# Optimization experiments

Measured on AMD Instinct MI355X. Metric: run time of the kernel, lower is better.

Reference implementation:

```python
import jax, jax.numpy as jnp
import numpy as np

B, L = 4, 1024
CS, CP, H, C = 384, 128, 8, 64
PQK, PV, RANK, K = 8, 12, 2, 10
CZ4 = CP // 4
ANG_TO_NM = 0.1
INF = 1e9


def layer_norm(x, g, b):
    m = jnp.mean(x, -1, keepdims=True)
    v = jnp.var(x, -1, keepdims=True)
    return (x - m) * jax.lax.rsqrt(v + 1e-5) * g + b


def quat_to_rot(q):
    w, x, y, z = q[..., 0], q[..., 1], q[..., 2], q[..., 3]
    R = jnp.stack([1 - 2 * (y * y + z * z), 2 * (x * y - w * z), 2 * (x * z + w * y),
                   2 * (x * y + w * z), 1 - 2 * (x * x + z * z), 2 * (y * z - w * x),
                   2 * (x * z - w * y), 2 * (y * z + w * x), 1 - 2 * (x * x + y * y)], -1)
    return R.reshape(q.shape[:-1] + (3, 3))


def pos_emb(n, dim):
    pos = jnp.arange(n, dtype=jnp.float32)[:, None]
    half = dim // 2
    freq = jnp.exp(-np.log(10000.0) / half * jnp.arange(half, dtype=jnp.float32))
    ang = pos * freq[None]
    return jnp.concatenate([jnp.sin(ang), jnp.cos(ang)], -1)


def forward(s, trans, rots, mask, We_s, be_s, We_mlp, be_mlp, Wf1, bf1, Wf2, bf2,
            Wq, Wk, Wv, Wqp, Wkp, Wvp, gamma, Wb1, Wb2, Wz1, Wz2, Wout, bout,
            ln1_g, ln1_b, Wt1, bt1, Wt2, bt2, Wt3, bt3, ln2_g, ln2_b, Wbb, bbb):
    b_, l_ = s.shape[0], s.shape[1]
    # ---- EdgeEmbedder (flash_1d_bias mode): per-node low-rank factors of pair rep,
    # with on-the-fly k-neighbor distance features; never materializes [L,L,c_p]. ----
    node = s @ We_s + be_s                                              # [B,L,CP]
    offs = np.concatenate([np.arange(-K, 0), np.arange(1, K + 1)])      # 2K seq neighbors
    idx = np.clip(np.arange(l_)[None, :] + offs[:, None], 0, l_ - 1)    # [2K,L]
    d = jnp.linalg.norm(trans[:, idx] - trans[:, None], axis=-1)        # [B,2K,L]
    d = jnp.moveaxis(d, 1, 2)                                           # [B,L,2K]
    pe = jnp.broadcast_to(pos_emb(l_, CP)[None], (b_, l_, CP))
    hmid = jax.nn.relu(jnp.concatenate([node, pe, d], -1) @ We_mlp + be_mlp)
    z1 = (hmid @ Wf1 + bf1).reshape(b_, l_, RANK, CP) * mask[..., None, None]
    z2 = (hmid @ Wf2 + bf2).reshape(b_, l_, RANK, CP) * mask[..., None, None]
    # ---- Invariant Point Attention on rigids (translations in nm) ----
    t_nm = trans * ANG_TO_NM
    q = (s @ Wq).reshape(b_, l_, H, C)
    k = (s @ Wk).reshape(b_, l_, H, C)
    v = (s @ Wv).reshape(b_, l_, H, C)
    qp = (s @ Wqp).reshape(b_, l_, H, PQK, 3)
    kp = (s @ Wkp).reshape(b_, l_, H, PQK, 3)
    vp = (s @ Wvp).reshape(b_, l_, H, PV, 3)

    def to_global(p):
        return jnp.einsum('blxy,blhpy->blhpx', rots, p) + t_nm[:, :, None, None, :]

    qp, kp, vp = to_global(qp), to_global(kp), to_global(vp)
    a = jnp.einsum('bihc,bjhc->bhij', q, k) * float(1.0 / np.sqrt(3 * C))
    # factored pair bias: b[h,i,j] = sum_r f1[i,r,h] * f2[j,r,h]
    bf_i = jnp.einsum('birc,ch->birh', z1, Wb1)
    bf_j = jnp.einsum('bjrc,ch->bjrh', z2, Wb2)
    a = a + float(np.sqrt(1.0 / 3.0)) * jnp.einsum('birh,bjrh->bhij', bf_i, bf_j)
    # point attention via |q|^2 + |k|^2 - 2 q.k (no [L,L,P,3] tensor)
    q2 = jnp.moveaxis((qp ** 2).sum((-2, -1)), -1, 1)                   # [B,H,L]
    k2 = jnp.moveaxis((kp ** 2).sum((-2, -1)), -1, 1)
    d2 = q2[..., None] + k2[:, :, None, :] - 2.0 * jnp.einsum('bihpx,bjhpx->bhij', qp, kp)
    head_w = jax.nn.softplus(gamma) * float(np.sqrt(1.0 / (3 * (PQK * 9.0 / 2))))
    a = a - 0.5 * head_w[None, :, None, None] * d2
    a = a + (mask[:, None, None, :] - 1.0) * INF
    a = jax.nn.softmax(a, -1)
    o = jnp.einsum('bhij,bjhc->bihc', a, v).reshape(b_, l_, H * C)
    og = jnp.einsum('bhij,bjhpx->bihpx', a, vp)
    op = jnp.einsum('blyx,blhpy->blhpx', rots, og - t_nm[:, :, None, None, :])
    opn = jnp.sqrt((op ** 2).sum(-1) + 1e-8)                            # [B,L,H,PV]
    # factored pair-value: o_pair[i] = z1v[i] * (a @ z2v)
    zv1 = jnp.einsum('birc,cd->bird', z1, Wz1)
    zv2 = jnp.einsum('bjrc,cd->bjrd', z2, Wz2)
    opair = zv1[:, :, None] * jnp.einsum('bhij,bjrd->bihrd', a, zv2)    # [B,L,H,R,CZ4]
    cat = jnp.concatenate([o, op.reshape(b_, l_, H * PV * 3), opn.reshape(b_, l_, H * PV),
                           opair.reshape(b_, l_, H * RANK * CZ4)], -1)
    s = s + cat @ Wout + bout
    s = layer_norm(s, ln1_g, ln1_b)
    # ---- structure transition (residual MLP + LN) ----
    h2 = jax.nn.relu(s @ Wt1 + bt1)
    h2 = jax.nn.relu(h2 @ Wt2 + bt2)
    s = layer_norm(s + h2 @ Wt3 + bt3, ln2_g, ln2_b)
    # ---- backbone update + rigid compose ----
    u = s @ Wbb + bbb                                                   # [B,L,6]
    quat = jnp.concatenate([jnp.ones(u.shape[:-1] + (1,), u.dtype), u[..., :3]], -1)
    quat = quat / jnp.linalg.norm(quat, axis=-1, keepdims=True)
    r_u = quat_to_rot(quat)
    rots_new = jnp.einsum('blxy,blyz->blxz', rots, r_u)
    trans_new = jnp.einsum('blxy,bly->blx', rots, u[..., 3:]) + trans
    return s, rots_new, trans_new


def setup_inputs() -> dict:
    key = jax.random.key(0)
    ks = jax.random.split(key, 40)

    def w(i, shape, scale=0.02):
        return jax.random.normal(ks[i], shape, jnp.float32) * scale

    s = jax.random.normal(ks[0], (B, L, CS), jnp.float32)
    trans = jax.random.normal(ks[1], (B, L, 3), jnp.float32) * 10.0
    qr = jax.random.normal(ks[2], (B, L, 4), jnp.float32)
    rots = quat_to_rot(qr / jnp.linalg.norm(qr, axis=-1, keepdims=True))
    mask = jnp.ones((B, L), jnp.float32)
    return dict(
        s=s, trans=trans, rots=rots, mask=mask,
        We_s=w(3, (CS, CP)), be_s=jnp.zeros((CP,)),
        We_mlp=w(4, (2 * CP + 2 * K, CP)), be_mlp=jnp.zeros((CP,)),
        Wf1=w(5, (CP, RANK * CP)), bf1=jnp.zeros((RANK * CP,)),
        Wf2=w(6, (CP, RANK * CP)), bf2=jnp.zeros((RANK * CP,)),
        Wq=w(7, (CS, H * C)), Wk=w(8, (CS, H * C)), Wv=w(9, (CS, H * C)),
        Wqp=w(10, (CS, H * PQK * 3)), Wkp=w(11, (CS, H * PQK * 3)), Wvp=w(12, (CS, H * PV * 3)),
        gamma=jnp.zeros((H,)), Wb1=w(13, (CP, H)), Wb2=w(14, (CP, H)),
        Wz1=w(15, (CP, CZ4)), Wz2=w(16, (CP, CZ4)),
        Wout=w(17, (H * (C + PV * 4) + H * RANK * CZ4, CS)), bout=jnp.zeros((CS,)),
        ln1_g=jnp.ones((CS,)), ln1_b=jnp.zeros((CS,)),
        Wt1=w(18, (CS, CS)), bt1=jnp.zeros((CS,)),
        Wt2=w(19, (CS, CS)), bt2=jnp.zeros((CS,)),
        Wt3=w(20, (CS, CS)), bt3=jnp.zeros((CS,)),
        ln2_g=jnp.ones((CS,)), ln2_b=jnp.zeros((CS,)),
        Wbb=w(21, (CS, 6)), bbb=jnp.zeros((6,)))


def reference(s, trans, rots, mask, We_s, be_s, We_mlp, be_mlp, Wf1, bf1, Wf2, bf2,
              Wq, Wk, Wv, Wqp, Wkp, Wvp, gamma, Wb1, Wb2, Wz1, Wz2, Wout, bout,
              ln1_g, ln1_b, Wt1, bt1, Wt2, bt2, Wt3, bt3, ln2_g, ln2_b, Wbb, bbb):
    return forward(s, trans, rots, mask, We_s, be_s, We_mlp, be_mlp, Wf1, bf1, Wf2, bf2,
                   Wq, Wk, Wv, Wqp, Wkp, Wvp, gamma, Wb1, Wb2, Wz1, Wz2, Wout, bout,
                   ln1_g, ln1_b, Wt1, bt1, Wt2, bt2, Wt3, bt3, ln2_g, ln2_b, Wbb, bbb)
```

## Files before the change

### kernel.cpp

```cpp
#include <hip/hip_runtime.h>
#include <math.h>

#define Bb 4
#define Ll 1024
#define CSd 384
#define CPd 128
#define Hh 8
#define BL 4096
#define CAT2W 276
#define CATW 1408
#define QKVW 2208
#define PARTW 168
#define LDP 40

#define S_QK 0.07216878364870322f
#define SQ13 0.5773502691896258f
#define HW_SCALE 0.09622504486493764f

typedef short bf16x8 __attribute__((ext_vector_type(8)));
typedef float f32x4  __attribute__((ext_vector_type(4)));

__device__ __forceinline__ ushort f2bf(float f) {
    uint u = __float_as_uint(f);
    u += 0x7FFF + ((u >> 16) & 1);
    return (ushort)(u >> 16);
}
__device__ __forceinline__ float bf2f(ushort h) {
    return __uint_as_float(((uint)h) << 16);
}

template<bool RELU, bool HASBIAS>
__global__ __launch_bounds__(256) void gemm_mfma(
    const float* __restrict__ A, int lda,
    const float* __restrict__ W, const float* __restrict__ bias,
    float* __restrict__ C, int ldc, int N, int Kd)
{
    __shared__ short Ah[64][LDP], Al[64][LDP];
    __shared__ short Wh[64][LDP], Wl[64][LDP];
    const int tid = threadIdx.x;
    const int lane = tid & 63;
    const int wave = tid >> 6;
    const int qm = wave >> 1, qn = wave & 1;
    const int bm = blockIdx.y * 64, bn = blockIdx.x * 64;

    f32x4 acc[2][2];
#pragma unroll
    for (int i = 0; i < 2; ++i)
#pragma unroll
        for (int j = 0; j < 2; ++j) {
            acc[i][j][0] = 0.f; acc[i][j][1] = 0.f;
            acc[i][j][2] = 0.f; acc[i][j][3] = 0.f;
        }

    const int rsel = lane & 15;
    const int ksel = (lane >> 4) * 8;

    for (int k0 = 0; k0 < Kd; k0 += 32) {
        __syncthreads();
        {
            const int row = tid >> 2, kc = (tid & 3) * 8;
            const float* ap = A + (size_t)(bm + row) * lda + k0 + kc;
            float av[8];
            if (k0 + kc + 8 <= Kd) {
                const float4 a0 = *(const float4*)ap;
                const float4 a1 = *(const float4*)(ap + 4);
                av[0]=a0.x; av[1]=a0.y; av[2]=a0.z; av[3]=a0.w;
                av[4]=a1.x; av[5]=a1.y; av[6]=a1.z; av[7]=a1.w;
            } else {
#pragma unroll
                for (int u = 0; u < 8; ++u)
                    av[u] = (k0 + kc + u < Kd) ? ap[u] : 0.f;
            }
            short hv[8], lv[8];
#pragma unroll
            for (int u = 0; u < 8; ++u) {
                const ushort h = f2bf(av[u]);
                hv[u] = (short)h;
                lv[u] = (short)f2bf(av[u] - bf2f(h));
            }
            *(bf16x8*)&Ah[row][kc] = *(const bf16x8*)hv;
            *(bf16x8*)&Al[row][kc] = *(const bf16x8*)lv;
        }
        {
            const int col = tid & 63, ko = (tid >> 6) * 8;
            const int swz = ((col >> 3) & 3) << 3;
            const bool cok = (bn + col) < N;
            float wv[8];
#pragma unroll
            for (int i = 0; i < 8; ++i) {
                const int k = k0 + ko + i;
                wv[i] = (cok && k < Kd) ? W[(size_t)k * N + bn + col] : 0.f;
            }
            short hv[8], lv[8];
#pragma unroll
            for (int i = 0; i < 8; ++i) {
                const ushort h = f2bf(wv[i]);
                hv[i] = (short)h;
                lv[i] = (short)f2bf(wv[i] - bf2f(h));
            }
            *(bf16x8*)&Wh[col][ko ^ swz] = *(const bf16x8*)hv;
            *(bf16x8*)&Wl[col][ko ^ swz] = *(const bf16x8*)lv;
        }
        __syncthreads();

        bf16x8 afh[2], afl[2], wfh[2], wfl[2];
#pragma unroll
        for (int fr = 0; fr < 2; ++fr) {
            const int row = qm * 32 + fr * 16 + rsel;
            afh[fr] = *(const bf16x8*)&Ah[row][ksel];
            afl[fr] = *(const bf16x8*)&Al[row][ksel];
        }
#pragma unroll
        for (int fc = 0; fc < 2; ++fc) {
            const int col = qn * 32 + fc * 16 + rsel;
            const int swz = ((col >> 3) & 3) << 3;
            wfh[fc] = *(const bf16x8*)&Wh[col][ksel ^ swz];
            wfl[fc] = *(const bf16x8*)&Wl[col][ksel ^ swz];
        }
#pragma unroll
        for (int fr = 0; fr < 2; ++fr)
#pragma unroll
            for (int fc = 0; fc < 2; ++fc) {
                acc[fr][fc] = __builtin_amdgcn_mfma_f32_16x16x32_bf16(
                    afh[fr], wfh[fc], acc[fr][fc], 0, 0, 0);
                acc[fr][fc] = __builtin_amdgcn_mfma_f32_16x16x32_bf16(
                    afh[fr], wfl[fc], acc[fr][fc], 0, 0, 0);
                acc[fr][fc] = __builtin_amdgcn_mfma_f32_16x16x32_bf16(
                    afl[fr], wfh[fc], acc[fr][fc], 0, 0, 0);
            }
    }

#pragma unroll
    for (int fr = 0; fr < 2; ++fr)
#pragma unroll
        for (int fc = 0; fc < 2; ++fc) {
            const int col = bn + qn * 32 + fc * 16 + rsel;
            if (col < N) {
                const float bv = HASBIAS ? bias[col] : 0.f;
#pragma unroll
                for (int r = 0; r < 4; ++r) {
                    const int row = bm + qm * 32 + fr * 16 + (lane >> 4) * 4 + r;
                    float x = acc[fr][fc][r] + bv;
                    if (RELU) x = fmaxf(x, 0.f);
                    C[(size_t)row * ldc + col] = x;
                }
            }
        }
}

__global__ __launch_bounds__(256) void pack_qkv(
    const float* __restrict__ Wq, const float* __restrict__ Wk,
    const float* __restrict__ Wv, const float* __restrict__ Wqp,
    const float* __restrict__ Wkp, const float* __restrict__ Wvp,
    float* __restrict__ Wp)
{
    const int k = blockIdx.x;
    float* dst = Wp + (size_t)k * QKVW;
    for (int n = threadIdx.x; n < QKVW; n += 256) {
        float v;
        if      (n < 512)  v = Wq [(size_t)k*512 + n];
        else if (n < 1024) v = Wk [(size_t)k*512 + n - 512];
        else if (n < 1536) v = Wv [(size_t)k*512 + n - 1024];
        else if (n < 1728) v = Wqp[(size_t)k*192 + n - 1536];
        else if (n < 1920) v = Wkp[(size_t)k*192 + n - 1728];
        else               v = Wvp[(size_t)k*288 + n - 1920];
        dst[n] = v;
    }
}

__global__ __launch_bounds__(256) void pack_f12(
    const float* __restrict__ Wf1, const float* __restrict__ Wf2,
    const float* __restrict__ bf1, const float* __restrict__ bf2,
    float* __restrict__ Wp, float* __restrict__ bp)
{
    const int k = blockIdx.x;
    float* dst = Wp + (size_t)k * 512;
    for (int n = threadIdx.x; n < 512; n += 256)
        dst[n] = (n < 256) ? Wf1[(size_t)k*256 + n] : Wf2[(size_t)k*256 + n - 256];
    if (k == 0)
        for (int n = threadIdx.x; n < 512; n += 256)
            bp[n] = (n < 256) ? bf1[n] : bf2[n - 256];
}

__global__ __launch_bounds__(128) void edge_feat(
    const float* __restrict__ trans, float* __restrict__ cat2)
{
    const int row = blockIdx.x;
    const int l = row & (Ll - 1);
    const int b = row >> 10;
    const int tid = threadIdx.x;
    {
        float v;
        if (tid < 64) {
            const float fr = __expf(-9.210340371976184f / 64.f * (float)tid);
            v = sinf((float)l * fr);
        } else {
            const float fr = __expf(-9.210340371976184f / 64.f * (float)(tid - 64));
            v = cosf((float)l * fr);
        }
        cat2[(size_t)row * CAT2W + 128 + tid] = v;
    }
    if (tid < 20) {
        const int off = (tid < 10) ? (tid - 10) : (tid - 9);
        int j = l + off;
        j = j < 0 ? 0 : (j > Ll - 1 ? Ll - 1 : j);
        const float dx = trans[(size_t)(b*Ll + j)*3 + 0] - trans[(size_t)row*3 + 0];
        const float dy = trans[(size_t)(b*Ll + j)*3 + 1] - trans[(size_t)row*3 + 1];
        const float dz = trans[(size_t)(b*Ll + j)*3 + 2] - trans[(size_t)row*3 + 2];
        cat2[(size_t)row * CAT2W + 256 + tid] = sqrtf(dx*dx + dy*dy + dz*dz);
    }
}

__global__ __launch_bounds__(256) void z_derive(
    const float* __restrict__ z12, const float* __restrict__ mask,
    const float* __restrict__ Wb1, const float* __restrict__ Wb2,
    const float* __restrict__ Wz1, const float* __restrict__ Wz2,
    float* __restrict__ bfi, float* __restrict__ bfj,
    float* __restrict__ zv1, float* __restrict__ zv2)
{
    __shared__ float zsh[512];
    const int row = blockIdx.x;
    const int tid = threadIdx.x;
    for (int idx = tid; idx < 512; idx += 256)
        zsh[idx] = z12[(size_t)row * 512 + idx];
    __syncthreads();
    const float mv = mask[row];
    if (tid < 16) {
        const int r = tid >> 3, h = tid & 7;
        float acc = 0.f;
        for (int c = 0; c < 128; ++c) acc = fmaf(zsh[r*128 + c], Wb1[c*8 + h], acc);
        bfi[(size_t)row*16 + r*8 + h] = mv * acc;
    } else if (tid < 80) {
        const int o = tid - 16, r = o >> 5, dd = o & 31;
        float acc = 0.f;
        for (int c = 0; c < 128; ++c) acc = fmaf(zsh[r*128 + c], Wz1[c*32 + dd], acc);
        zv1[(size_t)row*64 + r*32 + dd] = mv * acc;
    } else if (tid < 96) {
        const int o = tid - 80, r = o >> 3, h = o & 7;
        float acc = 0.f;
        for (int c = 0; c < 128; ++c) acc = fmaf(zsh[256 + r*128 + c], Wb2[c*8 + h], acc);
        bfj[(size_t)row*16 + r*8 + h] = mv * acc;
    } else if (tid < 160) {
        const int o = tid - 96, r = o >> 5, dd = o & 31;
        float acc = 0.f;
        for (int c = 0; c < 128; ++c) acc = fmaf(zsh[256 + r*128 + c], Wz2[c*32 + dd], acc);
        zv2[(size_t)row*64 + r*32 + dd] = mv * acc;
    }
}

__global__ __launch_bounds__(256) void to_global_k(
    const float* __restrict__ rots, const float* __restrict__ trans,
    float* __restrict__ qkv, float* __restrict__ q2, float* __restrict__ k2)
{
    const int row = blockIdx.x;
    const int b = row >> 10, l = row & (Ll - 1);
    const int tid = threadIdx.x;
    __shared__ float sq[64], sk[64];
    float R[9], tn[3];
#pragma unroll
    for (int i = 0; i < 9; ++i) R[i] = rots[(size_t)row*9 + i];
#pragma unroll
    for (int i = 0; i < 3; ++i) tn[i] = trans[(size_t)row*3 + i] * 0.1f;

    float* base = nullptr;
    float* sq2 = nullptr;
    if (tid < 64)       { base = qkv + (size_t)row*QKVW + 1536 + tid*3;        sq2 = &sq[tid]; }
    else if (tid < 128) { base = qkv + (size_t)row*QKVW + 1728 + (tid-64)*3;   sq2 = &sk[tid-64]; }
    else if (tid < 224) { base = qkv + (size_t)row*QKVW + 1920 + (tid-128)*3; }
    if (base) {
        const float px = base[0], py = base[1], pz = base[2];
        const float gx = fmaf(R[0],px, fmaf(R[1],py, fmaf(R[2],pz, tn[0])));
        const float gy = fmaf(R[3],px, fmaf(R[4],py, fmaf(R[5],pz, tn[1])));
        const float gz = fmaf(R[6],px, fmaf(R[7],py, fmaf(R[8],pz, tn[2])));
        base[0] = gx; base[1] = gy; base[2] = gz;
        if (sq2) *sq2 = gx*gx + gy*gy + gz*gz;
    }
    __syncthreads();
    if (tid < 8) {
        float s2 = 0.f;
#pragma unroll
        for (int p = 0; p < 8; ++p) s2 += sq[tid*8 + p];
        q2[((size_t)b*Hh + tid)*Ll + l] = s2;
    } else if (tid < 16) {
        const int h = tid - 8;
        float s2 = 0.f;
#pragma unroll
        for (int p = 0; p < 8; ++p) s2 += sk[h*8 + p];
        k2[((size_t)b*Hh + h)*Ll + l] = s2;
    }
}

__global__ __launch_bounds__(256, 2) void flash_ipa4(
    const float* __restrict__ qkv,
    const float* __restrict__ q2g, const float* __restrict__ k2g,
    const float* __restrict__ bfi, const float* __restrict__ bfj,
    const float* __restrict__ zv2,
    const float* __restrict__ maskg, const float* __restrict__ gamma,
    float* __restrict__ part)
{
    __shared__ float sk[32][64];
    __shared__ float skp[32][32];
    __shared__ float sv[32][64];
    __shared__ float svp[32][36];
    __shared__ float szv[32][64];
    __shared__ float4 sjs[32];

    const int tid = threadIdx.x;
    const int t = tid & 7, g = tid >> 3;
    const int jh = blockIdx.x & 1;
    const int it = (blockIdx.x >> 1) & 7;
    const int bh = blockIdx.x >> 4;
    const int b = bh >> 3, h = bh & 7;
    const int i0 = it * 128 + g;

    const float hw = log1pf(__expf(gamma[h])) * HW_SCALE;
    const float nh = -0.5f * hw;

    float qa[4][8], qp[4][4], cI[4], bfa[4], bfb[4];
#pragma unroll
    for (int rr = 0; rr < 4; ++rr) {
        const int row = b * Ll + i0 + 32 * rr;
        const float* p0 = qkv + (size_t)row * QKVW + h * 64 + 8 * t;
        const float4 a0 = *(const float4*)p0, a1 = *(const float4*)(p0 + 4);
        qa[rr][0]=a0.x*S_QK; qa[rr][1]=a0.y*S_QK; qa[rr][2]=a0.z*S_QK; qa[rr][3]=a0.w*S_QK;
        qa[rr][4]=a1.x*S_QK; qa[rr][5]=a1.y*S_QK; qa[rr][6]=a1.z*S_QK; qa[rr][7]=a1.w*S_QK;
        float4 e0 = make_float4(0,0,0,0);
        if (t < 6)
            e0 = *(const float4*)(qkv + (size_t)row*QKVW + 1536 + h*24 + 4*t);
        qp[rr][0]=e0.x*hw; qp[rr][1]=e0.y*hw; qp[rr][2]=e0.z*hw; qp[rr][3]=e0.w*hw;
        cI[rr]  = nh * q2g[((size_t)b*Hh + h)*Ll + i0 + 32*rr];
        bfa[rr] = SQ13 * bfi[(size_t)row*16 + h];
        bfb[rr] = SQ13 * bfi[(size_t)row*16 + 8 + h];
    }

    float o[4][8] = {}, og[4][5] = {}, op[4][8] = {};
    float m[4] = {-1e30f,-1e30f,-1e30f,-1e30f}, l[4] = {};

    for (int jt = jh * 16; jt < jh * 16 + 16; ++jt) {
        const int rowj = b * Ll + jt * 32;
        __syncthreads();
#pragma unroll
        for (int r = 0; r < 2; ++r) {
            const int idx = tid + 256 * r;
            const int jj = idx >> 4, c4 = idx & 15;
            const float* src = qkv + (size_t)(rowj + jj) * QKVW;
            *(float4*)&sk[jj][c4*4]  = *(const float4*)(src + 512  + h*64 + c4*4);
            *(float4*)&sv[jj][c4*4]  = *(const float4*)(src + 1024 + h*64 + c4*4);
            *(float4*)&szv[jj][c4*4] = *(const float4*)(zv2 + (size_t)(rowj + jj)*64 + c4*4);
        }
        {
            const int jj = tid >> 3, c4 = tid & 7;
            float4 v4 = make_float4(0,0,0,0);
            if (c4 < 6)
                v4 = *(const float4*)(qkv + (size_t)(rowj + jj)*QKVW + 1728 + h*24 + c4*4);
            *(float4*)&skp[jj][c4*4] = v4;
        }
#pragma unroll
        for (int r = 0; r < 2; ++r) {
            const int idx = tid + 256 * r;
            if (idx < 288) {
                const int jj = idx / 9, c4 = idx % 9;
                *(float4*)&svp[jj][c4*4] =
                    *(const float4*)(qkv + (size_t)(rowj + jj)*QKVW + 1920 + h*36 + c4*4);
            }
        }
        if (tid < 32) {
            const int j = jt * 32 + tid;
            sjs[tid] = make_float4(
                k2g[((size_t)b*Hh + h)*Ll + j],
                (maskg[(size_t)b*Ll + j] - 1.f) * 1e9f,
                bfj[(size_t)(b*Ll + j)*16 + h],
                bfj[(size_t)(b*Ll + j)*16 + 8 + h]);
        }
        __syncthreads();

        for (int jj = 0; jj < 32; ++jj) {
            const float4 ka = *(const float4*)&sk[jj][8*t];
            const float4 kb = *(const float4*)&sk[jj][8*t + 4];
            const float4 kp4 = *(const float4*)&skp[jj][4*t];
            const float kv[8] = {ka.x,ka.y,ka.z,ka.w,kb.x,kb.y,kb.z,kb.w};
            const float kpv[4] = {kp4.x,kp4.y,kp4.z,kp4.w};
            float d[4];
#pragma unroll
            for (int rr = 0; rr < 4; ++rr) {
                float dd = 0.f;
#pragma unroll
                for (int u = 0; u < 8; ++u) dd = fmaf(qa[rr][u], kv[u], dd);
#pragma unroll
                for (int u = 0; u < 4; ++u) dd = fmaf(qp[rr][u], kpv[u], dd);
                d[rr] = dd;
            }
#pragma unroll
            for (int rr = 0; rr < 4; ++rr) {
                d[rr] += __shfl_xor(d[rr], 1, 64);
                d[rr] += __shfl_xor(d[rr], 2, 64);
                d[rr] += __shfl_xor(d[rr], 4, 64);
            }
            const float4 js = sjs[jj];

            const float4 va = *(const float4*)&sv[jj][8*t];
            const float4 vb = *(const float4*)&sv[jj][8*t + 4];
            const float vv[8] = {va.x,va.y,va.z,va.w,vb.x,vb.y,vb.z,vb.w};
            const float4 vpa = *(const float4*)&svp[jj][4*t];
            const float vpv[4] = {vpa.x,vpa.y,vpa.z,vpa.w};
            const float vpe = svp[jj][32 + (t & 3)];
            const float vpes = (t < 4) ? vpe : 0.f;
            const float4 za = *(const float4*)&szv[jj][8*t];
            const float4 zb = *(const float4*)&szv[jj][8*t + 4];
            const float zz[8] = {za.x,za.y,za.z,za.w,zb.x,zb.y,zb.z,zb.w};

#pragma unroll
            for (int rr = 0; rr < 4; ++rr) {
                const float lg = d[rr] +
                    fmaf(bfa[rr], js.z, fmaf(bfb[rr], js.w, fmaf(nh, js.x, js.y + cI[rr])));
                if (lg > m[rr]) {
                    const float f = __expf(m[rr] - lg); m[rr] = lg; l[rr] *= f;
#pragma unroll
                    for (int u = 0; u < 8; ++u) o[rr][u] *= f;
#pragma unroll
                    for (int u = 0; u < 5; ++u) og[rr][u] *= f;
#pragma unroll
                    for (int u = 0; u < 8; ++u) op[rr][u] *= f;
                }
                const float p = __expf(lg - m[rr]); l[rr] += p;
#pragma unroll
                for (int u = 0; u < 8; ++u) o[rr][u] = fmaf(p, vv[u], o[rr][u]);
#pragma unroll
                for (int u = 0; u < 4; ++u) og[rr][u] = fmaf(p, vpv[u], og[rr][u]);
                og[rr][4] = fmaf(p, vpes, og[rr][4]);
#pragma unroll
                for (int u = 0; u < 8; ++u) op[rr][u] = fmaf(p, zz[u], op[rr][u]);
            }
        }
    }

#pragma unroll
    for (int rr = 0; rr < 4; ++rr) {
        float* pr = part + ((size_t)(bh * 2 + jh) * Ll + i0 + 32 * rr) * PARTW;
        *(float4*)&pr[8*t]     = make_float4(o[rr][0], o[rr][1], o[rr][2], o[rr][3]);
        *(float4*)&pr[8*t + 4] = make_float4(o[rr][4], o[rr][5], o[rr][6], o[rr][7]);
        *(float4*)&pr[64 + 4*t] = make_float4(og[rr][0], og[rr][1], og[rr][2], og[rr][3]);
        if (t < 4) pr[96 + t] = og[rr][4];
        *(float4*)&pr[100 + 8*t]     = make_float4(op[rr][0], op[rr][1], op[rr][2], op[rr][3]);
        *(float4*)&pr[100 + 8*t + 4] = make_float4(op[rr][4], op[rr][5], op[rr][6], op[rr][7]);
        if (t == 0) { pr[164] = m[rr]; pr[165] = l[rr]; }
    }
}

__global__ __launch_bounds__(256) void combine_ipa(
    const float* __restrict__ part,
    const float* __restrict__ zv1,
    const float* __restrict__ rots, const float* __restrict__ trans,
    float* __restrict__ cat)
{
    __shared__ float sog[64][36];
    const int tid = threadIdx.x;
    const int t = tid & 7, g = tid >> 3;
    const int it = blockIdx.x & 15;
    const int bh = blockIdx.x >> 4;
    const int b = bh >> 3, h = bh & 7;
    const int i0 = it * 64 + g;

#pragma unroll
    for (int rr = 0; rr < 2; ++rr) {
        const int i = i0 + rr * 32;
        const int row = b * Ll + i;
        const float* pA = part + ((size_t)(bh * 2 + 0) * Ll + i) * PARTW;
        const float* pB = part + ((size_t)(bh * 2 + 1) * Ll + i) * PARTW;
        const float mA = pA[164], mB = pB[164];
        const float m = fmaxf(mA, mB);
        const float wA = __expf(mA - m), wB = __expf(mB - m);
        const float l = fmaf(wA, pA[165], wB * pB[165]);
        const float sA = wA / l, sB = wB / l;

        float* crow = cat + (size_t)row * CATW;
        {
            const float4 a0 = *(const float4*)&pA[8*t];
            const float4 a1 = *(const float4*)&pA[8*t + 4];
            const float4 b0 = *(const float4*)&pB[8*t];
            const float4 b1 = *(const float4*)&pB[8*t + 4];
            *(float4*)&crow[h*64 + 8*t] = make_float4(
                fmaf(sA, a0.x, sB * b0.x), fmaf(sA, a0.y, sB * b0.y),
                fmaf(sA, a0.z, sB * b0.z), fmaf(sA, a0.w, sB * b0.w));
            *(float4*)&crow[h*64 + 8*t + 4] = make_float4(
                fmaf(sA, a1.x, sB * b1.x), fmaf(sA, a1.y, sB * b1.y),
                fmaf(sA, a1.z, sB * b1.z), fmaf(sA, a1.w, sB * b1.w));
        }
        {
            const float4 a0 = *(const float4*)&pA[100 + 8*t];
            const float4 a1 = *(const float4*)&pA[100 + 8*t + 4];
            const float4 b0 = *(const float4*)&pB[100 + 8*t];
            const float4 b1 = *(const float4*)&pB[100 + 8*t + 4];
            const float4 z0 = *(const float4*)&zv1[(size_t)row*64 + 8*t];
            const float4 z1 = *(const float4*)&zv1[(size_t)row*64 + 8*t + 4];
            *(float4*)&crow[896 + h*64 + 8*t] = make_float4(
                z0.x * fmaf(sA, a0.x, sB * b0.x), z0.y * fmaf(sA, a0.y, sB * b0.y),
                z0.z * fmaf(sA, a0.z, sB * b0.z), z0.w * fmaf(sA, a0.w, sB * b0.w));
            *(float4*)&crow[896 + h*64 + 8*t + 4] = make_float4(
                z1.x * fmaf(sA, a1.x, sB * b1.x), z1.y * fmaf(sA, a1.y, sB * b1.y),
                z1.z * fmaf(sA, a1.z, sB * b1.z), z1.w * fmaf(sA, a1.w, sB * b1.w));
        }
        {
            const float4 a0 = *(const float4*)&pA[64 + 4*t];
            const float4 b0 = *(const float4*)&pB[64 + 4*t];
            sog[g + rr*32][4*t + 0] = fmaf(sA, a0.x, sB * b0.x);
            sog[g + rr*32][4*t + 1] = fmaf(sA, a0.y, sB * b0.y);
            sog[g + rr*32][4*t + 2] = fmaf(sA, a0.z, sB * b0.z);
            sog[g + rr*32][4*t + 3] = fmaf(sA, a0.w, sB * b0.w);
            if (t < 4)
                sog[g + rr*32][32 + t] = fmaf(sA, pA[96 + t], sB * pB[96 + t]);
        }
    }
    __syncthreads();
    for (int idx = tid; idx < 64 * 12; idx += 256) {
        const int ri = idx / 12, p = idx % 12;
        const int rowi = b * Ll + it * 64 + ri;
        const float ox = sog[ri][p*3 + 0] - trans[(size_t)rowi*3 + 0] * 0.1f;
        const float oy = sog[ri][p*3 + 1] - trans[(size_t)rowi*3 + 1] * 0.1f;
        const float oz = sog[ri][p*3 + 2] - trans[(size_t)rowi*3 + 2] * 0.1f;
        const float* R = rots + (size_t)rowi * 9;
        const float opx = fmaf(R[0], ox, fmaf(R[3], oy, R[6] * oz));
        const float opy = fmaf(R[1], ox, fmaf(R[4], oy, R[7] * oz));
        const float opz = fmaf(R[2], ox, fmaf(R[5], oy, R[8] * oz));
        const size_t base = (size_t)rowi * CATW + 512 + h*36 + p*3;
        cat[base + 0] = opx; cat[base + 1] = opy; cat[base + 2] = opz;
        cat[(size_t)rowi * CATW + 800 + h*12 + p] =
            sqrtf(opx*opx + opy*opy + opz*opz + 1e-8f);
    }
}

__global__ __launch_bounds__(384) void add_ln(
    const float* __restrict__ x, const float* __restrict__ y,
    const float* __restrict__ gw, const float* __restrict__ bw,
    float* __restrict__ out)
{
    __shared__ float red[6];
    const int row = blockIdx.x;
    const int c = threadIdx.x;
    const float v = x[(size_t)row*CSd + c] + y[(size_t)row*CSd + c];
    float s = v;
#pragma unroll
    for (int off = 32; off; off >>= 1) s += __shfl_down(s, off, 64);
    if ((c & 63) == 0) red[c >> 6] = s;
    __syncthreads();
    float mean = 0.f;
#pragma unroll
    for (int w = 0; w < 6; ++w) mean += red[w];
    mean *= (1.f / CSd);
    __syncthreads();
    const float d = v - mean;
    float sq = d * d;
#pragma unroll
    for (int off = 32; off; off >>= 1) sq += __shfl_down(sq, off, 64);
    if ((c & 63) == 0) red[c >> 6] = sq;
    __syncthreads();
    float var = 0.f;
#pragma unroll
    for (int w = 0; w < 6; ++w) var += red[w];
    var *= (1.f / CSd);
    out[(size_t)row*CSd + c] = d * rsqrtf(var + 1e-5f) * gw[c] + bw[c];
}

__global__ __launch_bounds__(64) void backbone(
    const float* __restrict__ s2, const float* __restrict__ Wbb,
    const float* __restrict__ bbb, const float* __restrict__ rots,
    const float* __restrict__ trans,
    float* __restrict__ outR, float* __restrict__ outT)
{
    const int row = blockIdx.x;
    const int t = threadIdx.x;
    float part[6] = {};
    for (int c = t; c < CSd; c += 64) {
        const float sv = s2[(size_t)row*CSd + c];
#pragma unroll
        for (int j = 0; j < 6; ++j) part[j] = fmaf(sv, Wbb[c*6 + j], part[j]);
    }
#pragma unroll
    for (int j = 0; j < 6; ++j) {
#pragma unroll
        for (int off = 32; off; off >>= 1) part[j] += __shfl_down(part[j], off, 64);
    }
    if (t == 0) {
        float u[6];
#pragma unroll
        for (int j = 0; j < 6; ++j) u[j] = part[j] + bbb[j];
        const float inv = 1.f / sqrtf(1.f + u[0]*u[0] + u[1]*u[1] + u[2]*u[2]);
        const float w = inv, x = u[0]*inv, y = u[1]*inv, z = u[2]*inv;
        const float Ru[9] = {
            1.f - 2.f*(y*y + z*z), 2.f*(x*y - w*z), 2.f*(x*z + w*y),
            2.f*(x*y + w*z), 1.f - 2.f*(x*x + z*z), 2.f*(y*z - w*x),
            2.f*(x*z - w*y), 2.f*(y*z + w*x), 1.f - 2.f*(x*x + y*y)};
        float R[9];
#pragma unroll
        for (int i2 = 0; i2 < 9; ++i2) R[i2] = rots[(size_t)row*9 + i2];
#pragma unroll
        for (int xi = 0; xi < 3; ++xi)
#pragma unroll
            for (int zi = 0; zi < 3; ++zi)
                outR[(size_t)row*9 + xi*3 + zi] =
                    fmaf(R[xi*3+0], Ru[0+zi],
                    fmaf(R[xi*3+1], Ru[3+zi], R[xi*3+2] * Ru[6+zi]));
#pragma unroll
        for (int xi = 0; xi < 3; ++xi)
            outT[(size_t)row*3 + xi] =
                fmaf(R[xi*3+0], u[3],
                fmaf(R[xi*3+1], u[4], R[xi*3+2] * u[5])) +
                trans[(size_t)row*3 + xi];
    }
}

extern "C" void kernel_launch(void* const* d_in, const int* in_sizes, int n_in,
                              void* d_out, int out_size, void* d_ws, size_t ws_size,
                              hipStream_t stream)
{
    const float* s      = (const float*)d_in[0];
    const float* trans  = (const float*)d_in[1];
    const float* rots   = (const float*)d_in[2];
    const float* mask   = (const float*)d_in[3];
    const float* We_s   = (const float*)d_in[4];
    const float* be_s   = (const float*)d_in[5];
    const float* We_mlp = (const float*)d_in[6];
    const float* be_mlp = (const float*)d_in[7];
    const float* Wf1    = (const float*)d_in[8];
    const float* bf1    = (const float*)d_in[9];
    const float* Wf2    = (const float*)d_in[10];
    const float* bf2    = (const float*)d_in[11];
    const float* Wq     = (const float*)d_in[12];
    const float* Wk     = (const float*)d_in[13];
    const float* Wv     = (const float*)d_in[14];
    const float* Wqp    = (const float*)d_in[15];
    const float* Wkp    = (const float*)d_in[16];
    const float* Wvp    = (const float*)d_in[17];
    const float* gamma  = (const float*)d_in[18];
    const float* Wb1    = (const float*)d_in[19];
    const float* Wb2    = (const float*)d_in[20];
    const float* Wz1    = (const float*)d_in[21];
    const float* Wz2    = (const float*)d_in[22];
    const float* Wout   = (const float*)d_in[23];
    const float* bout   = (const float*)d_in[24];
    const float* ln1_g  = (const float*)d_in[25];
    const float* ln1_b  = (const float*)d_in[26];
    const float* Wt1    = (const float*)d_in[27];
    const float* bt1    = (const float*)d_in[28];
    const float* Wt2    = (const float*)d_in[29];
    const float* bt2    = (const float*)d_in[30];
    const float* Wt3    = (const float*)d_in[31];
    const float* bt3    = (const float*)d_in[32];
    const float* ln2_g  = (const float*)d_in[33];
    const float* ln2_b  = (const float*)d_in[34];
    const float* Wbb    = (const float*)d_in[35];
    const float* bbb    = (const float*)d_in[36];

    float* ws = (float*)d_ws;
    size_t off = 0;
    auto alloc = [&](size_t n) { float* p = ws + off; off += n; return p; };
    float* cat2  = alloc((size_t)BL * CAT2W);
    float* hmid  = alloc((size_t)BL * 128);
    float* z12   = alloc((size_t)BL * 512);
    float* bfi   = alloc((size_t)BL * 16);
    float* bfj   = alloc((size_t)BL * 16);
    float* zv1   = alloc((size_t)BL * 64);
    float* zv2   = alloc((size_t)BL * 64);
    float* qkv   = alloc((size_t)BL * QKVW);
    float* q2    = alloc((size_t)BL * 8);
    float* k2    = alloc((size_t)BL * 8);
    float* cat   = alloc((size_t)BL * CATW);
    float* tmp1  = alloc((size_t)BL * CSd);
    float* s1    = alloc((size_t)BL * CSd);
    float* Wpk   = alloc((size_t)CSd * QKVW);
    float* Wf12  = alloc((size_t)128 * 512);
    float* bf12  = alloc(512);
    float* partb = alloc((size_t)32 * 2 * Ll * PARTW);
    float* h1    = z12;
    float* h2b   = qkv;
    float* tmp2  = tmp1;

    float* outS = (float*)d_out;
    float* outR = outS + (size_t)BL * CSd;
    float* outT = outR + (size_t)BL * 9;

    pack_qkv<<<dim3(CSd), dim3(256), 0, stream>>>(Wq, Wk, Wv, Wqp, Wkp, Wvp, Wpk);
    pack_f12<<<dim3(128), dim3(256), 0, stream>>>(Wf1, Wf2, bf1, bf2, Wf12, bf12);

    gemm_mfma<false,true><<<dim3(2,64), dim3(256), 0, stream>>>(s, CSd, We_s, be_s, cat2, CAT2W, 128, CSd);
    edge_feat<<<dim3(BL), dim3(128), 0, stream>>>(trans, cat2);
    gemm_mfma<true,true><<<dim3(2,64), dim3(256), 0, stream>>>(cat2, CAT2W, We_mlp, be_mlp, hmid, 128, 128, CAT2W);
    gemm_mfma<false,true><<<dim3(8,64), dim3(256), 0, stream>>>(hmid, 128, Wf12, bf12, z12, 512, 512, 128);
    z_derive<<<dim3(BL), dim3(256), 0, stream>>>(z12, mask, Wb1, Wb2, Wz1, Wz2, bfi, bfj, zv1, zv2);

    gemm_mfma<false,false><<<dim3(35,64), dim3(256), 0, stream>>>(s, CSd, Wpk, nullptr, qkv, QKVW, QKVW, CSd);
    to_global_k<<<dim3(BL), dim3(256), 0, stream>>>(rots, trans, qkv, q2, k2);

    flash_ipa4<<<dim3(512), dim3(256), 0, stream>>>(
        qkv, q2, k2, bfi, bfj, zv2, mask, gamma, partb);
    combine_ipa<<<dim3(512), dim3(256), 0, stream>>>(partb, zv1, rots, trans, cat);

    gemm_mfma<false,true><<<dim3(6,64), dim3(256), 0, stream>>>(cat, CATW, Wout, bout, tmp1, CSd, CSd, CATW);
    add_ln<<<dim3(BL), dim3(384), 0, stream>>>(s, tmp1, ln1_g, ln1_b, s1);

    gemm_mfma<true,true><<<dim3(6,64), dim3(256), 0, stream>>>(s1, CSd, Wt1, bt1, h1, CSd, CSd, CSd);
    gemm_mfma<true,true><<<dim3(6,64), dim3(256), 0, stream>>>(h1, CSd, Wt2, bt2, h2b, CSd, CSd, CSd);
    gemm_mfma<false,true><<<dim3(6,64), dim3(256), 0, stream>>>(h2b, CSd, Wt3, bt3, tmp2, CSd, CSd, CSd);
    add_ln<<<dim3(BL), dim3(384), 0, stream>>>(s1, tmp2, ln2_g, ln2_b, outS);

    backbone<<<dim3(BL), dim3(64), 0, stream>>>(outS, Wbb, bbb, rots, trans, outR, outT);
}
```

Before: 807.7 us.

## Pre-split operands into bf16 hi/lo buffers before GEMMs

Moves the fp32-to-bf16 hi/lo split out of the GEMM inner loop into separate conversion kernels. Weights are transposed and split once per call, and activations are split before each GEMM. The GEMM then loads contiguous bf16x8 vectors straight into shared memory, which removes the strided scalar weight loads and the repeated per-tile conversion. In exchange it adds many extra kernel launches and extra global round trips for the converted activations, and it reuses workspace regions as aliases.

```diff
diff --git a/kernel.cpp b/kernel.cpp
--- a/kernel.cpp
+++ b/kernel.cpp
@@ -29,11 +29,69 @@
     return __uint_as_float(((uint)h) << 16);
 }
 
+__global__ __launch_bounds__(256) void convert_act(
+    const float* __restrict__ in, ushort* __restrict__ hi, ushort* __restrict__ lo,
+    int K, int Kpad, int total8)
+{
+    const int kpd8 = Kpad >> 3;
+    for (int idx = blockIdx.x * 256 + threadIdx.x; idx < total8; idx += gridDim.x * 256) {
+        const int row = idx / kpd8;
+        const int kc = (idx - row * kpd8) * 8;
+        const float* p = in + (size_t)row * K + kc;
+        float v[8];
+        if (kc + 8 <= K) {
+            const float4 a = *(const float4*)p, b = *(const float4*)(p + 4);
+            v[0]=a.x; v[1]=a.y; v[2]=a.z; v[3]=a.w;
+            v[4]=b.x; v[5]=b.y; v[6]=b.z; v[7]=b.w;
+        } else {
+#pragma unroll
+            for (int u = 0; u < 8; ++u) v[u] = (kc + u < K) ? p[u] : 0.f;
+        }
+        ushort h[8], l[8];
+#pragma unroll
+        for (int u = 0; u < 8; ++u) {
+            h[u] = f2bf(v[u]);
+            l[u] = f2bf(v[u] - bf2f(h[u]));
+        }
+        *(bf16x8*)&hi[(size_t)row * Kpad + kc] = *(const bf16x8*)h;
+        *(bf16x8*)&lo[(size_t)row * Kpad + kc] = *(const bf16x8*)l;
+    }
+}
+
+__global__ __launch_bounds__(256) void convert_wt(
+    const float* __restrict__ W, ushort* __restrict__ hi, ushort* __restrict__ lo,
+    int K, int N, int Kpad)
+{
+    __shared__ float t[32][65];
+    const int bn = blockIdx.x * 64, k0 = blockIdx.y * 32;
+    const int tid = threadIdx.x;
+    {
+        const int n = tid & 63, kk = tid >> 6;
+#pragma unroll
+        for (int r = 0; r < 8; ++r) {
+            const int k = k0 + r * 4 + kk;
+            t[r * 4 + kk][n] = (k < K && bn + n < N) ? W[(size_t)k * N + bn + n] : 0.f;
+        }
+    }
+    __syncthreads();
+    const int n2 = tid >> 2, kc = (tid & 3) * 8;
+    ushort h[8], l[8];
+#pragma unroll
+    for (int u = 0; u < 8; ++u) {
+        const float v = t[kc + u][n2];
+        h[u] = f2bf(v);
+        l[u] = f2bf(v - bf2f(h[u]));
+    }
+    *(bf16x8*)&hi[(size_t)(bn + n2) * Kpad + k0 + kc] = *(const bf16x8*)h;
+    *(bf16x8*)&lo[(size_t)(bn + n2) * Kpad + k0 + kc] = *(const bf16x8*)l;
+}
+
 template<bool RELU, bool HASBIAS>
-__global__ __launch_bounds__(256) void gemm_mfma(
-    const float* __restrict__ A, int lda,
-    const float* __restrict__ W, const float* __restrict__ bias,
-    float* __restrict__ C, int ldc, int N, int Kd)
+__global__ __launch_bounds__(256) void gemm_bf16(
+    const ushort* __restrict__ Ahi, const ushort* __restrict__ Alo, int Kpad,
+    const ushort* __restrict__ Whi, const ushort* __restrict__ Wlo,
+    const float* __restrict__ bias,
+    float* __restrict__ C, int ldc, int N)
 {
     __shared__ short Ah[64][LDP], Al[64][LDP];
     __shared__ short Wh[64][LDP], Wl[64][LDP];
@@ -54,53 +112,16 @@
 
     const int rsel = lane & 15;
     const int ksel = (lane >> 4) * 8;
-
-    for (int k0 = 0; k0 < Kd; k0 += 32) {
+    const int arow = tid >> 2, akc = (tid & 3) * 8;
+    const int wcol = tid & 63, wko = (tid >> 6) * 8;
+    const int wswz = ((wcol >> 3) & 3) << 3;
+
+    for (int k0 = 0; k0 < Kpad; k0 += 32) {
         __syncthreads();
-        {
-            const int row = tid >> 2, kc = (tid & 3) * 8;
-            const float* ap = A + (size_t)(bm + row) * lda + k0 + kc;
-            float av[8];
-            if (k0 + kc + 8 <= Kd) {
-                const float4 a0 = *(const float4*)ap;
-                const float4 a1 = *(const float4*)(ap + 4);
-                av[0]=a0.x; av[1]=a0.y; av[2]=a0.z; av[3]=a0.w;
-                av[4]=a1.x; av[5]=a1.y; av[6]=a1.z; av[7]=a1.w;
-            } else {
-#pragma unroll
-                for (int u = 0; u < 8; ++u)
-                    av[u] = (k0 + kc + u < Kd) ? ap[u] : 0.f;
-            }
-            short hv[8], lv[8];
-#pragma unroll
-            for (int u = 0; u < 8; ++u) {
-                const ushort h = f2bf(av[u]);
-                hv[u] = (short)h;
-                lv[u] = (short)f2bf(av[u] - bf2f(h));
-            }
-            *(bf16x8*)&Ah[row][kc] = *(const bf16x8*)hv;
-            *(bf16x8*)&Al[row][kc] = *(const bf16x8*)lv;
-        }
-        {
-            const int col = tid & 63, ko = (tid >> 6) * 8;
-            const int swz = ((col >> 3) & 3) << 3;
-            const bool cok = (bn + col) < N;
-            float wv[8];
-#pragma unroll
-            for (int i = 0; i < 8; ++i) {
-                const int k = k0 + ko + i;
-                wv[i] = (cok && k < Kd) ? W[(size_t)k * N + bn + col] : 0.f;
-            }
-            short hv[8], lv[8];
-#pragma unroll
-            for (int i = 0; i < 8; ++i) {
-                const ushort h = f2bf(wv[i]);
-                hv[i] = (short)h;
-                lv[i] = (short)f2bf(wv[i] - bf2f(h));
-            }
-            *(bf16x8*)&Wh[col][ko ^ swz] = *(const bf16x8*)hv;
-            *(bf16x8*)&Wl[col][ko ^ swz] = *(const bf16x8*)lv;
-        }
+        *(bf16x8*)&Ah[arow][akc] = *(const bf16x8*)&Ahi[(size_t)(bm + arow) * Kpad + k0 + akc];
+        *(bf16x8*)&Al[arow][akc] = *(const bf16x8*)&Alo[(size_t)(bm + arow) * Kpad + k0 + akc];
+        *(bf16x8*)&Wh[wcol][wko ^ wswz] = *(const bf16x8*)&Whi[(size_t)(bn + wcol) * Kpad + k0 + wko];
+        *(bf16x8*)&Wl[wcol][wko ^ wswz] = *(const bf16x8*)&Wlo[(size_t)(bn + wcol) * Kpad + k0 + wko];
         __syncthreads();
 
         bf16x8 afh[2], afl[2], wfh[2], wfl[2];
@@ -667,40 +688,83 @@
     float* cat   = alloc((size_t)BL * CATW);
     float* tmp1  = alloc((size_t)BL * CSd);
     float* s1    = alloc((size_t)BL * CSd);
-    float* Wpk   = alloc((size_t)CSd * QKVW);
-    float* Wf12  = alloc((size_t)128 * 512);
+    float* WpkF  = alloc((size_t)CSd * QKVW);
+    float* Wf12F = alloc((size_t)128 * 512);
     float* bf12  = alloc(512);
     float* partb = alloc((size_t)32 * 2 * Ll * PARTW);
-    float* h1    = z12;
-    float* h2b   = qkv;
-    float* tmp2  = tmp1;
+    auto allocU = [&](size_t nu) { ushort* p = (ushort*)(ws + off); off += (nu + 1) / 2; return p; };
+    ushort* WTes = allocU((size_t)128 * 384 * 2);
+    ushort* WTem = allocU((size_t)128 * 288 * 2);
+    ushort* WTf  = allocU((size_t)512 * 128 * 2);
+    ushort* WTpk = allocU((size_t)2240 * 384 * 2);
+    ushort* WTo  = allocU((size_t)384 * 1408 * 2);
+    ushort* WTt1 = allocU((size_t)384 * 384 * 2);
+    ushort* WTt2 = allocU((size_t)384 * 384 * 2);
+    ushort* WTt3 = allocU((size_t)384 * 384 * 2);
+
+    ushort* sp    = (ushort*)tmp1;
+    ushort* cat2p = (ushort*)cat;
+    ushort* hmidp = (ushort*)(cat + (size_t)BL * 288);
+    ushort* catp  = (ushort*)partb;
+    ushort* s1p   = (ushort*)tmp1;
+    ushort* h1p   = (ushort*)(partb + (size_t)BL * 1408);
+    ushort* h2p   = (ushort*)(partb + (size_t)BL * 1792);
+    float* h1   = z12;
+    float* h2b  = qkv;
+    float* tmp2 = tmp1;
 
     float* outS = (float*)d_out;
     float* outR = outS + (size_t)BL * CSd;
     float* outT = outR + (size_t)BL * 9;
 
-    pack_qkv<<<dim3(CSd), dim3(256), 0, stream>>>(Wq, Wk, Wv, Wqp, Wkp, Wvp, Wpk);
-    pack_f12<<<dim3(128), dim3(256), 0, stream>>>(Wf1, Wf2, bf1, bf2, Wf12, bf12);
-
-    gemm_mfma<false,true><<<dim3(2,64), dim3(256), 0, stream>>>(s, CSd, We_s, be_s, cat2, CAT2W, 128, CSd);
+    auto cagrid = [](int total8) { int g = (total8 + 255) / 256; return g > 2048 ? 2048 : g; };
+
+    pack_qkv<<<dim3(CSd), dim3(256), 0, stream>>>(Wq, Wk, Wv, Wqp, Wkp, Wvp, WpkF);
+    pack_f12<<<dim3(128), dim3(256), 0, stream>>>(Wf1, Wf2, bf1, bf2, Wf12F, bf12);
+
+    convert_wt<<<dim3(2, 12),  dim3(256), 0, stream>>>(We_s,  WTes, WTes + (size_t)128*384,  CSd,   128,  384);
+    convert_wt<<<dim3(2, 9),   dim3(256), 0, stream>>>(We_mlp,WTem, WTem + (size_t)128*288,  CAT2W, 128,  288);
+    convert_wt<<<dim3(8, 4),   dim3(256), 0, stream>>>(Wf12F, WTf,  WTf  + (size_t)512*128,  128,   512,  128);
+    convert_wt<<<dim3(35, 12), dim3(256), 0, stream>>>(WpkF,  WTpk, WTpk + (size_t)2240*384, CSd,   QKVW, 384);
+    convert_wt<<<dim3(6, 44),  dim3(256), 0, stream>>>(Wout,  WTo,  WTo  + (size_t)384*1408, CATW,  CSd,  1408);
+    convert_wt<<<dim3(6, 12),  dim3(256), 0, stream>>>(Wt1,   WTt1, WTt1 + (size_t)384*384,  CSd,   CSd,  384);
+    convert_wt<<<dim3(6, 12),  dim3(256), 0, stream>>>(Wt2,   WTt2, WTt2 + (size_t)384*384,  CSd,   CSd,  384);
+    convert_wt<<<dim3(6, 12),  dim3(256), 0, stream>>>(Wt3,   WTt3, WTt3 + (size_t)384*384,  CSd,   CSd,  384);
+
+    convert_act<<<dim3(cagrid(BL*48)), dim3(256), 0, stream>>>(s, sp, sp + (size_t)BL*384, CSd, 384, BL*48);
+    gemm_bf16<false,true><<<dim3(2,64), dim3(256), 0, stream>>>(
+        sp, sp + (size_t)BL*384, 384, WTes, WTes + (size_t)128*384, be_s, cat2, CAT2W, 128);
     edge_feat<<<dim3(BL), dim3(128), 0, stream>>>(trans, cat2);
-    gemm_mfma<true,true><<<dim3(2,64), dim3(256), 0, stream>>>(cat2, CAT2W, We_mlp, be_mlp, hmid, 128, 128, CAT2W);
-    gemm_mfma<false,true><<<dim3(8,64), dim3(256), 0, stream>>>(hmid, 128, Wf12, bf12, z12, 512, 512, 128);
+    convert_act<<<dim3(cagrid(BL*36)), dim3(256), 0, stream>>>(cat2, cat2p, cat2p + (size_t)BL*288, CAT2W, 288, BL*36);
+    gemm_bf16<true,true><<<dim3(2,64), dim3(256), 0, stream>>>(
+        cat2p, cat2p + (size_t)BL*288, 288, WTem, WTem + (size_t)128*288, be_mlp, hmid, 128, 128);
+    convert_act<<<dim3(cagrid(BL*16)), dim3(256), 0, stream>>>(hmid, hmidp, hmidp + (size_t)BL*128, 128, 128, BL*16);
+    gemm_bf16<false,true><<<dim3(8,64), dim3(256), 0, stream>>>(
+        hmidp, hmidp + (size_t)BL*128, 128, WTf, WTf + (size_t)512*128, bf12, z12, 512, 512);
     z_derive<<<dim3(BL), dim3(256), 0, stream>>>(z12, mask, Wb1, Wb2, Wz1, Wz2, bfi, bfj, zv1, zv2);
 
-    gemm_mfma<false,false><<<dim3(35,64), dim3(256), 0, stream>>>(s, CSd, Wpk, nullptr, qkv, QKVW, QKVW, CSd);
+    gemm_bf16<false,false><<<dim3(35,64), dim3(256), 0, stream>>>(
+        sp, sp + (size_t)BL*384, 384, WTpk, WTpk + (size_t)2240*384, nullptr, qkv, QKVW, QKVW);
     to_global_k<<<dim3(BL), dim3(256), 0, stream>>>(rots, trans, qkv, q2, k2);
 
     flash_ipa4<<<dim3(512), dim3(256), 0, stream>>>(
         qkv, q2, k2, bfi, bfj, zv2, mask, gamma, partb);
     combine_ipa<<<dim3(512), dim3(256), 0, stream>>>(partb, zv1, rots, trans, cat);
 
-    gemm_mfma<false,true><<<dim3(6,64), dim3(256), 0, stream>>>(cat, CATW, Wout, bout, tmp1, CSd, CSd, CATW);
+    convert_act<<<dim3(cagrid(BL*176)), dim3(256), 0, stream>>>(cat, catp, catp + (size_t)BL*1408, CATW, 1408, BL*176);
+    gemm_bf16<false,true><<<dim3(6,64), dim3(256), 0, stream>>>(
+        catp, catp + (size_t)BL*1408, 1408, WTo, WTo + (size_t)384*1408, bout, tmp1, CSd, CSd);
     add_ln<<<dim3(BL), dim3(384), 0, stream>>>(s, tmp1, ln1_g, ln1_b, s1);
 
-    gemm_mfma<true,true><<<dim3(6,64), dim3(256), 0, stream>>>(s1, CSd, Wt1, bt1, h1, CSd, CSd, CSd);
-    gemm_mfma<true,true><<<dim3(6,64), dim3(256), 0, stream>>>(h1, CSd, Wt2, bt2, h2b, CSd, CSd, CSd);
-    gemm_mfma<false,true><<<dim3(6,64), dim3(256), 0, stream>>>(h2b, CSd, Wt3, bt3, tmp2, CSd, CSd, CSd);
+    convert_act<<<dim3(cagrid(BL*48)), dim3(256), 0, stream>>>(s1, s1p, s1p + (size_t)BL*384, CSd, 384, BL*48);
+    gemm_bf16<true,true><<<dim3(6,64), dim3(256), 0, stream>>>(
+        s1p, s1p + (size_t)BL*384, 384, WTt1, WTt1 + (size_t)384*384, bt1, h1, CSd, CSd);
+    convert_act<<<dim3(cagrid(BL*48)), dim3(256), 0, stream>>>(h1, h1p, h1p + (size_t)BL*384, CSd, 384, BL*48);
+    gemm_bf16<true,true><<<dim3(6,64), dim3(256), 0, stream>>>(
+        h1p, h1p + (size_t)BL*384, 384, WTt2, WTt2 + (size_t)384*384, bt2, h2b, CSd, CSd);
+    convert_act<<<dim3(cagrid(BL*48)), dim3(256), 0, stream>>>(h2b, h2p, h2p + (size_t)BL*384, CSd, 384, BL*48);
+    gemm_bf16<false,true><<<dim3(6,64), dim3(256), 0, stream>>>(
+        h2p, h2p + (size_t)BL*384, 384, WTt3, WTt3 + (size_t)384*384, bt3, tmp2, CSd, CSd);
     add_ln<<<dim3(BL), dim3(384), 0, stream>>>(s1, tmp2, ln2_g, ln2_b, outS);
 
     backbone<<<dim3(BL), dim3(64), 0, stream>>>(outS, Wbb, bbb, rots, trans, outR, outT);
```

New measurement: 826.7 us. +2.3%, slower.
